# Optimization experiments

Measured on AMD Instinct MI355X. Metric: run time of the kernel, lower is better.

Reference implementation:

```python
import jax, jax.numpy as jnp
import numpy as np

N_NODES = 50000
N_EDGES = 800000
NFEAT = 128
NHID = 64  # gc1: NFEAT -> 2*NHID, gc2: 2*NHID -> NHID


def setup_inputs() -> dict:
    key = jax.random.key(0)
    k1, k2, k3, k4, k5 = jax.random.split(key, 5)
    feat = jax.random.normal(k1, (N_NODES, NFEAT), dtype=jnp.float32)
    src = jax.random.randint(k2, (N_EDGES,), 0, N_NODES, dtype=jnp.int32)
    dst = jax.random.randint(k3, (N_EDGES,), 0, N_NODES, dtype=jnp.int32)
    # GraphConv weights: (in_feats, out_feats), xavier-like scale
    W1 = jax.random.normal(k4, (NFEAT, 2 * NHID), dtype=jnp.float32) / np.sqrt(NFEAT)
    b1 = jnp.zeros((2 * NHID,), dtype=jnp.float32)
    W2 = jax.random.normal(k5, (2 * NHID, NHID), dtype=jnp.float32) / np.sqrt(2 * NHID)
    b2 = jnp.zeros((NHID,), dtype=jnp.float32)
    return {"feat": feat, "src": src, "dst": dst, "W1": W1, "b1": b1, "W2": W2, "b2": b2}


def _graph_conv(feat, src, dst, W, b):
    """DGL GraphConv, norm='both', allow_zero_in_degree=True.
    h = D_in^{-1/2} A (D_out^{-1/2} x) W + b, with degrees clamped to >= 1.
    Applies W before aggregation when in_feats > out_feats (saves bandwidth)."""
    N = feat.shape[0]
    ones = jnp.ones(src.shape[0], dtype=feat.dtype)
    deg_out = jnp.clip(jax.ops.segment_sum(ones, src, num_segments=N), 1.0)
    deg_in = jnp.clip(jax.ops.segment_sum(ones, dst, num_segments=N), 1.0)
    h = feat * (deg_out ** -0.5)[:, None]
    mult_first = W.shape[0] > W.shape[1]
    if mult_first:
        h = h @ W
    agg = jax.ops.segment_sum(h[src], dst, num_segments=N)  # [N, d]
    if not mult_first:
        agg = agg @ W
    return agg * (deg_in ** -0.5)[:, None] + b


def reference(feat, src, dst, W1, b1, W2, b2):
    x = jax.nn.relu(_graph_conv(feat, src, dst, W1, b1))
    # dropout is inactive in eval mode (F.dropout training=False)
    x = _graph_conv(x, src, dst, W2, b2)
    return jax.nn.log_softmax(x, axis=1)
```

## Files before the change

### kernel.cpp

```cpp
#include <hip/hip_runtime.h>
#include <math.h>


constexpr int NF   = 128;
constexpr int NH   = 64;
constexpr int CAP  = 48;
constexpr int EPB  = 4096;
constexpr int BCAP = 8192;
constexpr int NBKMAX = 256;

typedef unsigned int uint;
typedef unsigned short ushort_t;
typedef __attribute__((ext_vector_type(8))) short short8;
typedef __attribute__((ext_vector_type(4))) float f32x4;

__device__ __forceinline__ float bflo(uint u) { return __uint_as_float(u << 16); }
__device__ __forceinline__ float bfhi(uint u) { return __uint_as_float(u & 0xffff0000u); }
__device__ __forceinline__ uint packbf(float a, float b) {
    uint ua = __float_as_uint(a), ub = __float_as_uint(b);
    uint ra = (ua + 0x7fffu + ((ua >> 16) & 1u)) >> 16;
    uint rb = (ub + 0x7fffu + ((ub >> 16) & 1u)) >> 16;
    return ra | (rb << 16);
}
__device__ __forceinline__ ushort_t bf16u(float f) {
    uint u = __float_as_uint(f);
    return (ushort_t)((u + 0x7fffu + ((u >> 16) & 1u)) >> 16);
}
__device__ __forceinline__ short8 as_short8(uint4 u) {
    union { uint4 u; short8 s; } x; x.u = u; return x.s;
}

__global__ __launch_bounds__(1024) void partition_kernel(
        const int* __restrict__ src, const int* __restrict__ dst,
        int2* __restrict__ pairs_g, int* __restrict__ srcb_g,
        int* __restrict__ dcur, int* __restrict__ scur,
        int E, int nbk) {
    __shared__ int2 pl[EPB];
    __shared__ int  sl[EPB];
    __shared__ int  dh[NBKMAX], sh[NBKMAX];
    __shared__ int  doff[NBKMAX], soff[NBKMAX];
    __shared__ int  dbase[NBKMAX], sbase[NBKMAX];
    __shared__ int  dpos[NBKMAX], spos[NBKMAX];
    int tid = threadIdx.x;
    int e0 = blockIdx.x * EPB;
    int ecnt = min(EPB, E - e0);

    for (int b = tid; b < nbk; b += 1024) { dh[b] = 0; sh[b] = 0; }
    __syncthreads();
    for (int i = tid; i < ecnt; i += 1024) {
        atomicAdd(&dh[dst[e0 + i] >> 8], 1);
        atomicAdd(&sh[src[e0 + i] >> 8], 1);
    }
    __syncthreads();
    if (tid == 0)  { int run = 0; for (int b = 0; b < nbk; ++b) { doff[b] = run; run += dh[b]; } }
    if (tid == 64) { int run = 0; for (int b = 0; b < nbk; ++b) { soff[b] = run; run += sh[b]; } }
    for (int b = tid; b < nbk; b += 1024) {
        dbase[b] = atomicAdd(&dcur[b], dh[b]);
        sbase[b] = atomicAdd(&scur[b], sh[b]);
    }
    __syncthreads();
    for (int b = tid; b < nbk; b += 1024) { dpos[b] = doff[b]; spos[b] = soff[b]; }
    __syncthreads();
    for (int i = tid; i < ecnt; i += 1024) {
        int s = src[e0 + i], d = dst[e0 + i];
        int p = atomicAdd(&dpos[d >> 8], 1);
        pl[p] = make_int2(s, d);
        int q = atomicAdd(&spos[s >> 8], 1);
        sl[q] = s;
    }
    __syncthreads();
    for (int i = tid; i < ecnt; i += 1024) {
        int2 e = pl[i];
        int b = e.y >> 8;
        int gp = dbase[b] + (i - doff[b]);
        if (gp < BCAP) pairs_g[(size_t)b * BCAP + gp] = e;
        int sv = sl[i];
        int b2 = sv >> 8;
        int gq = sbase[b2] + (i - soff[b2]);
        if (gq < BCAP) srcb_g[(size_t)b2 * BCAP + gq] = sv;
    }
}

__global__ __launch_bounds__(1024) void bin_kernel(
        const int2* __restrict__ pairs_g, const int* __restrict__ srcb_g,
        const int* __restrict__ dcur, const int* __restrict__ scur,
        int* __restrict__ slots, int* __restrict__ lens,
        float* __restrict__ s_in, float* __restrict__ s_out, int N) {
    __shared__ int slots_l[256 * CAP];
    __shared__ int cin[256], cout[256];
    int tid = threadIdx.x;
    int b = blockIdx.x;
    int lo = b << 8;
    for (int r = tid; r < 256; r += 1024) { cin[r] = 0; cout[r] = 0; }
    __syncthreads();
    int dn = min(dcur[b], BCAP);
    for (int i = tid; i < dn; i += 1024) {
        int2 e = pairs_g[(size_t)b * BCAP + i];
        int r = e.y - lo;
        int p = atomicAdd(&cin[r], 1);
        if (p < CAP) slots_l[r * CAP + p] = e.x;
    }
    int sn = min(scur[b], BCAP);
    for (int i = tid; i < sn; i += 1024)
        atomicAdd(&cout[srcb_g[(size_t)b * BCAP + i] - lo], 1);
    __syncthreads();
    int nrow = min(256, N - lo);
    int lim4 = nrow * (CAP / 4);
    const int4* sl4 = (const int4*)slots_l;
    int4* gs4 = (int4*)(slots + (size_t)lo * CAP);
    for (int k = tid; k < 256 * CAP / 4; k += 1024)
        if (k < lim4) gs4[k] = sl4[k];
    for (int r = tid; r < nrow; r += 1024) {
        int node = lo + r;
        int ci = cin[r];
        lens[node]  = min(ci, CAP);
        s_in[node]  = rsqrtf((float)max(ci, 1));
        s_out[node] = rsqrtf((float)max(cout[r], 1));
    }
}

__global__ __launch_bounds__(256) void cast_feat_kernel(
        const float* __restrict__ feat, const float* __restrict__ s_out,
        uint* __restrict__ featb, int total8) {
    int i = blockIdx.x * 256 + threadIdx.x;
    if (i >= total8) return;
    int row = i >> 4;
    float sc = s_out[row];
    const float4* f4 = (const float4*)feat + (size_t)i * 2;
    float4 a = f4[0], b = f4[1];
    uint4 o;
    o.x = packbf(a.x * sc, a.y * sc);
    o.y = packbf(a.z * sc, a.w * sc);
    o.z = packbf(b.x * sc, b.y * sc);
    o.w = packbf(b.z * sc, b.w * sc);
    ((uint4*)featb)[i] = o;
}

__global__ __launch_bounds__(256) void cast_w_kernel(
        const float* __restrict__ W1, const float* __restrict__ W2,
        uint* __restrict__ W1p, uint* __restrict__ W2p) {
    int i = blockIdx.x * 256 + threadIdx.x;
    if (i < 8192) {
        int jp = i & 3, g = (i >> 2) & 3, n = (i >> 4) & 127, kk = i >> 11;
        int k = kk * 32 + g * 8 + jp * 2;
        W1p[i] = packbf(W1[k * 128 + n], W1[(k + 1) * 128 + n]);
    } else if (i < 12288) {
        int j = i - 8192;
        int jp = j & 3, g = (j >> 2) & 3, n = (j >> 4) & 63, kk = j >> 10;
        int k = kk * 32 + g * 8 + jp * 2;
        W2p[j] = packbf(W2[k * 64 + n], W2[(k + 1) * 64 + n]);
    }
}

__global__ __launch_bounds__(256) void agg1_kernel(const uint* __restrict__ featb,
        const int* __restrict__ lens, const int* __restrict__ slots,
        uint* __restrict__ agg1b, int N) {
    int wave = threadIdx.x >> 6;
    int lane = threadIdx.x & 63;
    int q   = lane >> 4;
    int sub = lane & 15;
    int node = blockIdx.x * 4 + wave;
    if (node >= N) return;
    int beg = node * CAP;
    int len = lens[node];
    float acc[8] = {0.f, 0.f, 0.f, 0.f, 0.f, 0.f, 0.f, 0.f};
    if (len > 0) {
        int li = min(lane, len - 1);
        int sidx = slots[beg + li];
        int quads = (len + 3) >> 2;
        #pragma unroll 4
        for (int k = 0; k < quads; ++k) {
            int e = 4 * k + q;
            int s = __shfl(sidx, e, 64);
            if (e < len) {
                uint4 v = *(const uint4*)(featb + (size_t)s * 64 + sub * 4);
                acc[0] += bflo(v.x); acc[1] += bfhi(v.x);
                acc[2] += bflo(v.y); acc[3] += bfhi(v.y);
                acc[4] += bflo(v.z); acc[5] += bfhi(v.z);
                acc[6] += bflo(v.w); acc[7] += bfhi(v.w);
            }
        }
    }
    #pragma unroll
    for (int j = 0; j < 8; ++j) {
        acc[j] += __shfl_xor(acc[j], 32, 64);
        acc[j] += __shfl_xor(acc[j], 16, 64);
    }
    if (q == 0) {
        uint4 o;
        o.x = packbf(acc[0], acc[1]);
        o.y = packbf(acc[2], acc[3]);
        o.z = packbf(acc[4], acc[5]);
        o.w = packbf(acc[6], acc[7]);
        *(uint4*)(agg1b + (size_t)node * 64 + sub * 4) = o;
    }
}

__global__ __launch_bounds__(256) void fused_gemm_kernel(
        const uint* __restrict__ agg1b, const uint* __restrict__ W1p,
        const float* __restrict__ b1, const uint* __restrict__ W2p,
        const float* __restrict__ s_in, const float* __restrict__ s_out,
        uint* __restrict__ h2b, int N) {
    __shared__ ushort_t x1t[64][136];
    __shared__ float sin_l[64], sout_l[64];
    int t = threadIdx.x;
    int base = blockIdx.x * 64;
    int w    = t >> 6;
    int lane = t & 63;
    int c = lane & 15;
    int g = lane >> 4;

    if (t < 64)       sin_l[t]        = (base + t < N) ? s_in[base + t] : 0.f;
    else if (t < 128) sout_l[t - 64]  = (base + t - 64 < N) ? s_out[base + t - 64] : 0.f;
    __syncthreads();

    f32x4 zero = {0.f, 0.f, 0.f, 0.f};
    f32x4 c1[4][2];
    #pragma unroll
    for (int mt = 0; mt < 4; ++mt) { c1[mt][0] = zero; c1[mt][1] = zero; }
    #pragma unroll
    for (int kk = 0; kk < 4; ++kk) {
        short8 bf[2];
        #pragma unroll
        for (int ntl = 0; ntl < 2; ++ntl) {
            int n = (2 * w + ntl) * 16 + c;
            bf[ntl] = as_short8(*(const uint4*)(W1p + (size_t)kk * 2048 + n * 16 + g * 4));
        }
        #pragma unroll
        for (int mt = 0; mt < 4; ++mt) {
            int row = base + mt * 16 + c;
            short8 af = as_short8(*(const uint4*)(agg1b + (size_t)row * 64 + kk * 16 + g * 4));
            c1[mt][0] = __builtin_amdgcn_mfma_f32_16x16x32_bf16(af, bf[0], c1[mt][0], 0, 0, 0);
            c1[mt][1] = __builtin_amdgcn_mfma_f32_16x16x32_bf16(af, bf[1], c1[mt][1], 0, 0, 0);
        }
    }
    float bias0 = b1[(2 * w) * 16 + c];
    float bias1 = b1[(2 * w + 1) * 16 + c];
    #pragma unroll
    for (int mt = 0; mt < 4; ++mt) {
        #pragma unroll
        for (int r = 0; r < 4; ++r) {
            int rl = mt * 16 + g * 4 + r;
            float si = sin_l[rl], so = sout_l[rl];
            x1t[rl][(2 * w) * 16 + c]     = bf16u(fmaxf(fmaf(si, c1[mt][0][r], bias0), 0.f) * so);
            x1t[rl][(2 * w + 1) * 16 + c] = bf16u(fmaxf(fmaf(si, c1[mt][1][r], bias1), 0.f) * so);
        }
    }
    __syncthreads();

    f32x4 c2[4];
    #pragma unroll
    for (int mt = 0; mt < 4; ++mt) c2[mt] = zero;
    #pragma unroll
    for (int kk = 0; kk < 4; ++kk) {
        int n = w * 16 + c;
        short8 bf2 = as_short8(*(const uint4*)(W2p + (size_t)kk * 1024 + n * 16 + g * 4));
        #pragma unroll
        for (int mt = 0; mt < 4; ++mt) {
            short8 af = *(const short8*)&x1t[mt * 16 + c][kk * 32 + g * 8];
            c2[mt] = __builtin_amdgcn_mfma_f32_16x16x32_bf16(af, bf2, c2[mt], 0, 0, 0);
        }
    }
    __syncthreads();

    ushort_t* h2t = &x1t[0][0];
    #pragma unroll
    for (int mt = 0; mt < 4; ++mt) {
        #pragma unroll
        for (int r = 0; r < 4; ++r) {
            int rl = mt * 16 + g * 4 + r;
            h2t[rl * 72 + w * 16 + c] = bf16u(c2[mt][r]);
        }
    }
    __syncthreads();
    int row = t >> 2, ch = t & 3;
    if (base + row < N) {
        uint4 v0 = *(const uint4*)(h2t + row * 72 + ch * 16);
        uint4 v1 = *(const uint4*)(h2t + row * 72 + ch * 16 + 8);
        *(uint4*)(h2b + (size_t)(base + row) * 32 + ch * 8)     = v0;
        *(uint4*)(h2b + (size_t)(base + row) * 32 + ch * 8 + 4) = v1;
    }
}

__global__ __launch_bounds__(256) void agg2_softmax_kernel(const uint* __restrict__ h2b,
        const int* __restrict__ lens, const int* __restrict__ slots,
        const float* __restrict__ s_in, const float* __restrict__ b2,
        float* __restrict__ out, int N) {
    int wave = threadIdx.x >> 6;
    int lane = threadIdx.x & 63;
    int oct = lane >> 3;
    int sub = lane & 7;
    int node = blockIdx.x * 4 + wave;
    if (node >= N) return;
    int beg = node * CAP;
    int len = lens[node];
    float acc[8] = {0.f, 0.f, 0.f, 0.f, 0.f, 0.f, 0.f, 0.f};
    if (len > 0) {
        int li = min(lane, len - 1);
        int sidx = slots[beg + li];
        int octs = (len + 7) >> 3;
        #pragma unroll 4
        for (int k = 0; k < octs; ++k) {
            int e = 8 * k + oct;
            int s = __shfl(sidx, e, 64);
            if (e < len) {
                uint4 v = *(const uint4*)(h2b + (size_t)s * 32 + sub * 4);
                acc[0] += bflo(v.x); acc[1] += bfhi(v.x);
                acc[2] += bflo(v.y); acc[3] += bfhi(v.y);
                acc[4] += bflo(v.z); acc[5] += bfhi(v.z);
                acc[6] += bflo(v.w); acc[7] += bfhi(v.w);
            }
        }
    }
    #pragma unroll
    for (int j = 0; j < 8; ++j) {
        acc[j] += __shfl_xor(acc[j], 32, 64);
        acc[j] += __shfl_xor(acc[j], 16, 64);
        acc[j] += __shfl_xor(acc[j], 8, 64);
    }
    float si = s_in[node];
    float4 bb0 = *(const float4*)(b2 + sub * 8);
    float4 bb1 = *(const float4*)(b2 + sub * 8 + 4);
    float v[8];
    v[0] = fmaf(acc[0], si, bb0.x); v[1] = fmaf(acc[1], si, bb0.y);
    v[2] = fmaf(acc[2], si, bb0.z); v[3] = fmaf(acc[3], si, bb0.w);
    v[4] = fmaf(acc[4], si, bb1.x); v[5] = fmaf(acc[5], si, bb1.y);
    v[6] = fmaf(acc[6], si, bb1.z); v[7] = fmaf(acc[7], si, bb1.w);

    float m = v[0];
    #pragma unroll
    for (int j = 1; j < 8; ++j) m = fmaxf(m, v[j]);
    m = fmaxf(m, __shfl_xor(m, 4, 64));
    m = fmaxf(m, __shfl_xor(m, 2, 64));
    m = fmaxf(m, __shfl_xor(m, 1, 64));
    float s8 = 0.f;
    #pragma unroll
    for (int j = 0; j < 8; ++j) s8 += expf(v[j] - m);
    s8 += __shfl_xor(s8, 4, 64);
    s8 += __shfl_xor(s8, 2, 64);
    s8 += __shfl_xor(s8, 1, 64);
    float ls = m + logf(s8);
    if (oct == 0) {
        float4 o0 = make_float4(v[0] - ls, v[1] - ls, v[2] - ls, v[3] - ls);
        float4 o1 = make_float4(v[4] - ls, v[5] - ls, v[6] - ls, v[7] - ls);
        *(float4*)(out + (size_t)node * NH + sub * 8)     = o0;
        *(float4*)(out + (size_t)node * NH + sub * 8 + 4) = o1;
    }
}

extern "C" void kernel_launch(void* const* d_in, const int* in_sizes, int n_in,
                              void* d_out, int out_size, void* d_ws, size_t ws_size,
                              hipStream_t stream) {
    const float* feat = (const float*)d_in[0];
    const int*   src  = (const int*)d_in[1];
    const int*   dst  = (const int*)d_in[2];
    const float* W1   = (const float*)d_in[3];
    const float* b1   = (const float*)d_in[4];
    const float* W2   = (const float*)d_in[5];
    const float* b2   = (const float*)d_in[6];
    float* out = (float*)d_out;

    int N = in_sizes[0] / NF;
    int E = in_sizes[1];
    int nbk = (N + 255) >> 8;
    int nchunk = (E + EPB - 1) / EPB;
    int Npad = (N + 63) & ~63;

    char* p = (char*)d_ws;
    auto alloc = [&](size_t bytes) -> char* {
        char* q = p;
        p += (bytes + 255) & ~(size_t)255;
        return q;
    };
    int*  dcur  = (int*)alloc((size_t)nbk * 4);
    int*  scur  = (int*)alloc((size_t)nbk * 4);
    int2* pairs = (int2*)alloc((size_t)nbk * BCAP * 8);
    int*  srcb  = (int*)alloc((size_t)nbk * BCAP * 4);
    int*  slots = (int*)alloc((size_t)N * CAP * 4);
    int*  lens  = (int*)alloc((size_t)N * 4);
    float* s_out = (float*)alloc((size_t)N * 4);
    float* s_in  = (float*)alloc((size_t)N * 4);
    uint*  featb = (uint*)alloc((size_t)N * 64 * 4);
    uint*  agg1b = (uint*)alloc((size_t)Npad * 64 * 4);
    uint*  W1p   = (uint*)alloc(8192 * 4);
    uint*  W2p   = (uint*)alloc(4096 * 4);
    uint*  h2b   = (uint*)alloc((size_t)N * 32 * 4);

    size_t cur_span = (size_t)((char*)scur - (char*)dcur) + (size_t)nbk * 4;
    hipMemsetAsync(dcur, 0, cur_span, stream);

    partition_kernel<<<nchunk, 1024, 0, stream>>>(src, dst, pairs, srcb, dcur, scur, E, nbk);
    bin_kernel<<<nbk, 1024, 0, stream>>>(pairs, srcb, dcur, scur, slots, lens, s_in, s_out, N);
    int total8 = N * 16;
    cast_feat_kernel<<<(total8 + 255) / 256, 256, 0, stream>>>(feat, s_out, featb, total8);
    cast_w_kernel<<<48, 256, 0, stream>>>(W1, W2, W1p, W2p);
    agg1_kernel<<<(N + 3) / 4, 256, 0, stream>>>(featb, lens, slots, agg1b, N);
    fused_gemm_kernel<<<(N + 63) / 64, 256, 0, stream>>>(agg1b, W1p, b1, W2p, s_in, s_out, h2b, N);
    agg2_softmax_kernel<<<(N + 3) / 4, 256, 0, stream>>>(h2b, lens, slots, s_in, b2, out, N);
}
```

Before: 180.5 us.

## Compress edge and slot indices to 16-bit and fuse feature cast into binning

Destination/source pairs are packed into one 32-bit word and the per-node neighbor slots and source bins are stored as 16-bit indices. This halves the index traffic in partitioning, binning and both aggregation kernels. The separate feature-cast kernel is folded into the bin kernel, which now scales and converts its 256 rows of features after computing out-degrees. The partition kernel moves to 2048 edges per block with 512 threads. Because the destination bucket is no longer stored with the edge, it is recovered by a binary search over the bucket offsets, which adds per-edge work. There is also a leftover dead loop and an unused second binary search. The 16-bit indices only hold for node counts below 65536.

Measured after the change: 183.1 us. About the same (+1.5%).

```diff
diff --git a/kernel.cpp b/kernel.cpp
--- a/kernel.cpp
+++ b/kernel.cpp
@@ -5,7 +5,8 @@
 constexpr int NF   = 128;
 constexpr int NH   = 64;
 constexpr int CAP  = 48;
-constexpr int EPB  = 4096;
+constexpr int EPB  = 2048;
+constexpr int PTH  = 512;
 constexpr int BCAP = 8192;
 constexpr int NBKMAX = 256;
 
@@ -30,64 +31,85 @@
     union { uint4 u; short8 s; } x; x.u = u; return x.s;
 }
 
-__global__ __launch_bounds__(1024) void partition_kernel(
+__global__ __launch_bounds__(PTH) void partition_kernel(
         const int* __restrict__ src, const int* __restrict__ dst,
-        int2* __restrict__ pairs_g, int* __restrict__ srcb_g,
+        uint* __restrict__ pairs_g, ushort_t* __restrict__ srcb_g,
         int* __restrict__ dcur, int* __restrict__ scur,
         int E, int nbk) {
-    __shared__ int2 pl[EPB];
-    __shared__ int  sl[EPB];
-    __shared__ int  dh[NBKMAX], sh[NBKMAX];
-    __shared__ int  doff[NBKMAX], soff[NBKMAX];
-    __shared__ int  dbase[NBKMAX], sbase[NBKMAX];
-    __shared__ int  dpos[NBKMAX], spos[NBKMAX];
+    __shared__ uint     pl[EPB];
+    __shared__ ushort_t sl[EPB];
+    __shared__ int dh[NBKMAX], sh[NBKMAX];
+    __shared__ int doff[NBKMAX], soff[NBKMAX];
+    __shared__ int dbase[NBKMAX], sbase[NBKMAX];
+    __shared__ int dpos[NBKMAX], spos[NBKMAX];
     int tid = threadIdx.x;
     int e0 = blockIdx.x * EPB;
     int ecnt = min(EPB, E - e0);
 
-    for (int b = tid; b < nbk; b += 1024) { dh[b] = 0; sh[b] = 0; }
-    __syncthreads();
-    for (int i = tid; i < ecnt; i += 1024) {
+    for (int b = tid; b < nbk; b += PTH) { dh[b] = 0; sh[b] = 0; }
+    __syncthreads();
+    for (int i = tid; i < ecnt; i += PTH) {
         atomicAdd(&dh[dst[e0 + i] >> 8], 1);
         atomicAdd(&sh[src[e0 + i] >> 8], 1);
     }
     __syncthreads();
     if (tid == 0)  { int run = 0; for (int b = 0; b < nbk; ++b) { doff[b] = run; run += dh[b]; } }
     if (tid == 64) { int run = 0; for (int b = 0; b < nbk; ++b) { soff[b] = run; run += sh[b]; } }
-    for (int b = tid; b < nbk; b += 1024) {
+    for (int b = tid; b < nbk; b += PTH) {
         dbase[b] = atomicAdd(&dcur[b], dh[b]);
         sbase[b] = atomicAdd(&scur[b], sh[b]);
     }
     __syncthreads();
-    for (int b = tid; b < nbk; b += 1024) { dpos[b] = doff[b]; spos[b] = soff[b]; }
-    __syncthreads();
-    for (int i = tid; i < ecnt; i += 1024) {
+    for (int b = tid; b < nbk; b += PTH) { dpos[b] = doff[b]; spos[b] = soff[b]; }
+    __syncthreads();
+    for (int i = tid; i < ecnt; i += PTH) {
         int s = src[e0 + i], d = dst[e0 + i];
         int p = atomicAdd(&dpos[d >> 8], 1);
-        pl[p] = make_int2(s, d);
+        pl[p] = ((uint)s << 8) | (uint)(d & 255);
         int q = atomicAdd(&spos[s >> 8], 1);
-        sl[q] = s;
-    }
-    __syncthreads();
-    for (int i = tid; i < ecnt; i += 1024) {
-        int2 e = pl[i];
-        int b = e.y >> 8;
+        sl[q] = (ushort_t)s;
+    }
+    __syncthreads();
+    for (int i = tid; i < ecnt; i += PTH) {
+        uint e = pl[i];
+        int b = (int)(e >> 16);
+        b = -1;
+        (void)b;
+        break;
+    }
+    __syncthreads();
+    for (int i = tid; i < ecnt; i += PTH) {
+        uint e = pl[i];
+        int loi = 0, hii = nbk - 1;
+        while (loi < hii) {
+            int mid = (loi + hii + 1) >> 1;
+            if (doff[mid] <= i) loi = mid; else hii = mid - 1;
+        }
+        int b = loi;
         int gp = dbase[b] + (i - doff[b]);
         if (gp < BCAP) pairs_g[(size_t)b * BCAP + gp] = e;
-        int sv = sl[i];
+        ushort_t sv = sl[i];
         int b2 = sv >> 8;
+        int loj = 0, hij = nbk - 1;
+        while (loj < hij) {
+            int mid = (loj + hij + 1) >> 1;
+            if (soff[mid] <= i) loj = mid; else hij = mid - 1;
+        }
+        (void)loj; (void)hij;
         int gq = sbase[b2] + (i - soff[b2]);
         if (gq < BCAP) srcb_g[(size_t)b2 * BCAP + gq] = sv;
     }
 }
 
 __global__ __launch_bounds__(1024) void bin_kernel(
-        const int2* __restrict__ pairs_g, const int* __restrict__ srcb_g,
+        const uint* __restrict__ pairs_g, const ushort_t* __restrict__ srcb_g,
         const int* __restrict__ dcur, const int* __restrict__ scur,
-        int* __restrict__ slots, int* __restrict__ lens,
+        const float* __restrict__ feat, uint* __restrict__ featb,
+        ushort_t* __restrict__ slots, int* __restrict__ lens,
         float* __restrict__ s_in, float* __restrict__ s_out, int N) {
-    __shared__ int slots_l[256 * CAP];
+    __shared__ ushort_t slots_l[256 * CAP];
     __shared__ int cin[256], cout[256];
+    __shared__ float souts[256];
     int tid = threadIdx.x;
     int b = blockIdx.x;
     int lo = b << 8;
@@ -95,45 +117,45 @@
     __syncthreads();
     int dn = min(dcur[b], BCAP);
     for (int i = tid; i < dn; i += 1024) {
-        int2 e = pairs_g[(size_t)b * BCAP + i];
-        int r = e.y - lo;
+        uint e = pairs_g[(size_t)b * BCAP + i];
+        int r = (int)(e & 255u);
         int p = atomicAdd(&cin[r], 1);
-        if (p < CAP) slots_l[r * CAP + p] = e.x;
+        if (p < CAP) slots_l[r * CAP + p] = (ushort_t)(e >> 8);
     }
     int sn = min(scur[b], BCAP);
     for (int i = tid; i < sn; i += 1024)
-        atomicAdd(&cout[srcb_g[(size_t)b * BCAP + i] - lo], 1);
+        atomicAdd(&cout[(int)srcb_g[(size_t)b * BCAP + i] - lo], 1);
     __syncthreads();
     int nrow = min(256, N - lo);
-    int lim4 = nrow * (CAP / 4);
-    const int4* sl4 = (const int4*)slots_l;
-    int4* gs4 = (int4*)(slots + (size_t)lo * CAP);
-    for (int k = tid; k < 256 * CAP / 4; k += 1024)
-        if (k < lim4) gs4[k] = sl4[k];
+    {
+        const uint4* sl4 = (const uint4*)slots_l;
+        uint4* gs4 = (uint4*)(slots + (size_t)lo * CAP);
+        int lim4 = nrow * (CAP / 8);
+        for (int k = tid; k < 256 * CAP / 8; k += 1024)
+            if (k < lim4) gs4[k] = sl4[k];
+    }
     for (int r = tid; r < nrow; r += 1024) {
         int node = lo + r;
         int ci = cin[r];
         lens[node]  = min(ci, CAP);
         s_in[node]  = rsqrtf((float)max(ci, 1));
-        s_out[node] = rsqrtf((float)max(cout[r], 1));
-    }
-}
-
-__global__ __launch_bounds__(256) void cast_feat_kernel(
-        const float* __restrict__ feat, const float* __restrict__ s_out,
-        uint* __restrict__ featb, int total8) {
-    int i = blockIdx.x * 256 + threadIdx.x;
-    if (i >= total8) return;
-    int row = i >> 4;
-    float sc = s_out[row];
-    const float4* f4 = (const float4*)feat + (size_t)i * 2;
-    float4 a = f4[0], b = f4[1];
-    uint4 o;
-    o.x = packbf(a.x * sc, a.y * sc);
-    o.y = packbf(a.z * sc, a.w * sc);
-    o.z = packbf(b.x * sc, b.y * sc);
-    o.w = packbf(b.z * sc, b.w * sc);
-    ((uint4*)featb)[i] = o;
+        float so    = rsqrtf((float)max(cout[r], 1));
+        s_out[node] = so;
+        souts[r]    = so;
+    }
+    __syncthreads();
+    for (int k = tid; k < nrow * 16; k += 1024) {
+        int r = k >> 4, ch = k & 15;
+        float sc = souts[r];
+        const float4* f4 = (const float4*)(feat + (size_t)(lo + r) * NF + ch * 8);
+        float4 a = f4[0], c = f4[1];
+        uint4 o;
+        o.x = packbf(a.x * sc, a.y * sc);
+        o.y = packbf(a.z * sc, a.w * sc);
+        o.z = packbf(c.x * sc, c.y * sc);
+        o.w = packbf(c.z * sc, c.w * sc);
+        *(uint4*)(featb + (size_t)(lo + r) * 64 + ch * 4) = o;
+    }
 }
 
 __global__ __launch_bounds__(256) void cast_w_kernel(
@@ -153,7 +175,7 @@
 }
 
 __global__ __launch_bounds__(256) void agg1_kernel(const uint* __restrict__ featb,
-        const int* __restrict__ lens, const int* __restrict__ slots,
+        const int* __restrict__ lens, const ushort_t* __restrict__ slots,
         uint* __restrict__ agg1b, int N) {
     int wave = threadIdx.x >> 6;
     int lane = threadIdx.x & 63;
@@ -166,7 +188,7 @@
     float acc[8] = {0.f, 0.f, 0.f, 0.f, 0.f, 0.f, 0.f, 0.f};
     if (len > 0) {
         int li = min(lane, len - 1);
-        int sidx = slots[beg + li];
+        int sidx = (int)slots[beg + li];
         int quads = (len + 3) >> 2;
         #pragma unroll 4
         for (int k = 0; k < quads; ++k) {
@@ -283,7 +305,7 @@
 }
 
 __global__ __launch_bounds__(256) void agg2_softmax_kernel(const uint* __restrict__ h2b,
-        const int* __restrict__ lens, const int* __restrict__ slots,
+        const int* __restrict__ lens, const ushort_t* __restrict__ slots,
         const float* __restrict__ s_in, const float* __restrict__ b2,
         float* __restrict__ out, int N) {
     int wave = threadIdx.x >> 6;
@@ -297,7 +319,7 @@
     float acc[8] = {0.f, 0.f, 0.f, 0.f, 0.f, 0.f, 0.f, 0.f};
     if (len > 0) {
         int li = min(lane, len - 1);
-        int sidx = slots[beg + li];
+        int sidx = (int)slots[beg + li];
         int octs = (len + 7) >> 3;
         #pragma unroll 4
         for (int k = 0; k < octs; ++k) {
@@ -372,28 +394,27 @@
         p += (bytes + 255) & ~(size_t)255;
         return q;
     };
-    int*  dcur  = (int*)alloc((size_t)nbk * 4);
-    int*  scur  = (int*)alloc((size_t)nbk * 4);
-    int2* pairs = (int2*)alloc((size_t)nbk * BCAP * 8);
-    int*  srcb  = (int*)alloc((size_t)nbk * BCAP * 4);
-    int*  slots = (int*)alloc((size_t)N * CAP * 4);
-    int*  lens  = (int*)alloc((size_t)N * 4);
-    float* s_out = (float*)alloc((size_t)N * 4);
-    float* s_in  = (float*)alloc((size_t)N * 4);
-    uint*  featb = (uint*)alloc((size_t)N * 64 * 4);
-    uint*  agg1b = (uint*)alloc((size_t)Npad * 64 * 4);
-    uint*  W1p   = (uint*)alloc(8192 * 4);
-    uint*  W2p   = (uint*)alloc(4096 * 4);
-    uint*  h2b   = (uint*)alloc((size_t)N * 32 * 4);
+    int*      dcur  = (int*)alloc((size_t)nbk * 4);
+    int*      scur  = (int*)alloc((size_t)nbk * 4);
+    uint*     pairs = (uint*)alloc((size_t)nbk * BCAP * 4);
+    ushort_t* srcb  = (ushort_t*)alloc((size_t)nbk * BCAP * 2);
+    ushort_t* slots = (ushort_t*)alloc((size_t)N * CAP * 2);
+    int*      lens  = (int*)alloc((size_t)N * 4);
+    float*    s_out = (float*)alloc((size_t)N * 4);
+    float*    s_in  = (float*)alloc((size_t)N * 4);
+    uint*     featb = (uint*)alloc((size_t)N * 64 * 4);
+    uint*     agg1b = (uint*)alloc((size_t)Npad * 64 * 4);
+    uint*     W1p   = (uint*)alloc(8192 * 4);
+    uint*     W2p   = (uint*)alloc(4096 * 4);
+    uint*     h2b   = (uint*)alloc((size_t)N * 32 * 4);
 
     size_t cur_span = (size_t)((char*)scur - (char*)dcur) + (size_t)nbk * 4;
     hipMemsetAsync(dcur, 0, cur_span, stream);
 
-    partition_kernel<<<nchunk, 1024, 0, stream>>>(src, dst, pairs, srcb, dcur, scur, E, nbk);
-    bin_kernel<<<nbk, 1024, 0, stream>>>(pairs, srcb, dcur, scur, slots, lens, s_in, s_out, N);
-    int total8 = N * 16;
-    cast_feat_kernel<<<(total8 + 255) / 256, 256, 0, stream>>>(feat, s_out, featb, total8);
+    partition_kernel<<<nchunk, PTH, 0, stream>>>(src, dst, pairs, srcb, dcur, scur, E, nbk);
     cast_w_kernel<<<48, 256, 0, stream>>>(W1, W2, W1p, W2p);
+    bin_kernel<<<nbk, 1024, 0, stream>>>(pairs, srcb, dcur, scur, feat, featb,
+                                         slots, lens, s_in, s_out, N);
     agg1_kernel<<<(N + 3) / 4, 256, 0, stream>>>(featb, lens, slots, agg1b, N);
     fused_gemm_kernel<<<(N + 63) / 64, 256, 0, stream>>>(agg1b, W1p, b1, W2p, s_in, s_out, h2b, N);
     agg2_softmax_kernel<<<(N + 3) / 4, 256, 0, stream>>>(h2b, lens, slots, s_in, b2, out, N);
```
